# Optimization experiments

Hardware: AMD Instinct MI355X
Metric: run time of the kernel (lower is better)

The kernel has to match this reference:

```python
import jax, jax.numpy as jnp
import numpy as np

B, N, ND, ED = 4, 24, 13, 12          # batch, num_nodes, node feat dim, edge feat dim
H, NH, HD = 256, 8, 32                # hidden, heads, head dim (H == NH*HD)
L, T = 64, 1000                       # transformer layers, max_timestep
_SCALE = 1.0 / float(np.sqrt(H))      # torch divides by sqrt(node_dim)=sqrt(256)


def _ln(x, g, b):
    m = x.mean(-1, keepdims=True)
    v = ((x - m) ** 2).mean(-1, keepdims=True)
    return (x - m) / jnp.sqrt(v + 1e-5) * g + b


def setup_inputs() -> dict:
    key = jax.random.key(0)
    it = iter(jax.random.split(key, 40))
    def w(*s):
        return (jax.random.normal(next(it), s) * 0.02).astype(jnp.float32)
    z = lambda *s: jnp.zeros(s, jnp.float32)
    o = lambda *s: jnp.ones(s, jnp.float32)
    d = {}
    d['nodes'] = jax.random.normal(next(it), (B, N, ND), jnp.float32)
    d['edges'] = jax.random.normal(next(it), (B, N, N, ED), jnp.float32)
    d['conds'] = jax.random.randint(next(it), (B,), 0, T)
    # input MLPs
    d['inN_w1'] = w(ND, H); d['inN_b1'] = z(H); d['inN_w2'] = w(H, H); d['inN_b2'] = z(H)
    d['inE_w1'] = w(ED, H); d['inE_b1'] = z(H); d['inE_w2'] = w(H, H); d['inE_b2'] = z(H)
    d['inC_w1'] = w(T, H);  d['inC_b1'] = z(H); d['inC_w2'] = w(H, H); d['inC_b2'] = z(H)
    # stacked per-layer params (leading dim L, scanned)
    d['qkv_w'] = w(L, H, 3 * H); d['qkv_b'] = z(L, 3 * H)
    d['no_w'] = w(L, H, H); d['no_b'] = z(L, H)
    d['eo_w'] = w(L, H, H); d['eo_b'] = z(L, H)
    d['ln1n_g'] = o(L, H); d['ln1n_b'] = z(L, H)
    d['ln1e_g'] = o(L, H); d['ln1e_b'] = z(L, H)
    d['mn_w1'] = w(L, H, 4 * H); d['mn_b1'] = z(L, 4 * H)
    d['mn_w2'] = w(L, 4 * H, H); d['mn_b2'] = z(L, H)
    d['me_w1'] = w(L, H, 4 * H); d['me_b1'] = z(L, 4 * H)
    d['me_w2'] = w(L, 4 * H, H); d['me_b2'] = z(L, H)
    d['ln2n_g'] = o(L, H); d['ln2n_b'] = z(L, H)
    d['ln2e_g'] = o(L, H); d['ln2e_b'] = z(L, H)
    # output MLPs
    d['outN_w1'] = w(H, H); d['outN_b1'] = z(H); d['outN_w2'] = w(H, ND); d['outN_b2'] = z(ND)
    d['outE_w1'] = w(H, H); d['outE_b1'] = z(H); d['outE_w2'] = w(H, ED); d['outE_b2'] = z(ED)
    return d


def _forward(nodes, edges, conds,
             inN_w1, inN_b1, inN_w2, inN_b2, inE_w1, inE_b1, inE_w2, inE_b2,
             inC_w1, inC_b1, inC_w2, inC_b2,
             qkv_w, qkv_b, no_w, no_b, eo_w, eo_b,
             ln1n_g, ln1n_b, ln1e_g, ln1e_b,
             mn_w1, mn_b1, mn_w2, mn_b2, me_w1, me_b1, me_w2, me_b2,
             ln2n_g, ln2n_b, ln2e_g, ln2e_b,
             outN_w1, outN_b1, outN_w2, outN_b2, outE_w1, outE_b1, outE_w2, outE_b2):
    relu = jax.nn.relu
    c = jax.nn.one_hot(conds, T, dtype=nodes.dtype)
    c = relu(relu(c @ inC_w1 + inC_b1) @ inC_w2 + inC_b2)          # (B,H)
    n = relu(relu(nodes @ inN_w1 + inN_b1) @ inN_w2 + inN_b2)      # (B,N,H)
    e = relu(relu(edges @ inE_w1 + inE_b1) @ inE_w2 + inE_b2)      # (B,N,N,H)

    def layer(carry, p):
        n, e = carry
        (qw, qb, nw, nb, ew, eb, g1n, b1n, g1e, b1e,
         w1n, bb1n, w2n, bb2n, w1e, bb1e, w2e, bb2e, g2n, b2n, g2e, b2e) = p
        nc = n + c[:, None, :]
        q, k, v = jnp.split(nc @ qw + qb, 3, axis=-1)
        q = q.reshape(B, N, NH, HD); k = k.reshape(B, N, NH, HD); v = v.reshape(B, N, NH, HD)
        s5 = jnp.einsum('bihd,bjhd->bijhd', q, k) * _SCALE          # (B,N,N,NH,HD)
        ne5 = s5 + e.reshape(B, N, N, NH, HD)                       # edge-biased scores
        attn = jax.nn.softmax(ne5.sum(-1), axis=2)                  # (B,N,N,NH)
        wv = jnp.einsum('bijh,bjhd->bihd', attn, v).reshape(B, N, H)
        an = _ln(wv @ nw + nb + n, g1n, b1n)
        ae = _ln(relu(ne5.reshape(B, N, N, H) @ ew + eb) + e, g1e, b1e)
        n2 = _ln(relu(an @ w1n + bb1n) @ w2n + bb2n + an, g2n, b2n)
        e2 = _ln(relu(ae @ w1e + bb1e) @ w2e + bb2e + ae, g2e, b2e)
        return (n2, e2), None

    stacked = (qkv_w, qkv_b, no_w, no_b, eo_w, eo_b, ln1n_g, ln1n_b, ln1e_g, ln1e_b,
               mn_w1, mn_b1, mn_w2, mn_b2, me_w1, me_b1, me_w2, me_b2,
               ln2n_g, ln2n_b, ln2e_g, ln2e_b)
    (n, e), _ = jax.lax.scan(layer, (n, e), stacked)
    out_n = relu(n @ outN_w1 + outN_b1) @ outN_w2 + outN_b2
    out_e = relu(e @ outE_w1 + outE_b1) @ outE_w2 + outE_b2
    return out_n, out_e


def reference(nodes, edges, conds,
              inN_w1, inN_b1, inN_w2, inN_b2, inE_w1, inE_b1, inE_w2, inE_b2,
              inC_w1, inC_b1, inC_w2, inC_b2,
              qkv_w, qkv_b, no_w, no_b, eo_w, eo_b,
              ln1n_g, ln1n_b, ln1e_g, ln1e_b,
              mn_w1, mn_b1, mn_w2, mn_b2, me_w1, me_b1, me_w2, me_b2,
              ln2n_g, ln2n_b, ln2e_g, ln2e_b,
              outN_w1, outN_b1, outN_w2, outN_b2, outE_w1, outE_b1, outE_w2, outE_b2):
    return _forward(nodes, edges, conds,
                    inN_w1, inN_b1, inN_w2, inN_b2, inE_w1, inE_b1, inE_w2, inE_b2,
                    inC_w1, inC_b1, inC_w2, inC_b2,
                    qkv_w, qkv_b, no_w, no_b, eo_w, eo_b,
                    ln1n_g, ln1n_b, ln1e_g, ln1e_b,
                    mn_w1, mn_b1, mn_w2, mn_b2, me_w1, me_b1, me_w2, me_b2,
                    ln2n_g, ln2n_b, ln2e_g, ln2e_b,
                    outN_w1, outN_b1, outN_w2, outN_b2, outE_w1, outE_b1, outE_w2, outE_b2)
```

## Files before the change

### kernel.cpp

```cpp
#include <hip/hip_runtime.h>

typedef _Float16 half_t;
typedef _Float16 f16x8 __attribute__((ext_vector_type(8)));
typedef _Float16 f16x4 __attribute__((ext_vector_type(4)));
typedef float f32x4 __attribute__((ext_vector_type(4)));

#define BB 4
#define NNODE 24
#define NLAYER 64
#define SCALE_QK 0.0625f

#define WS_C     0
#define WS_N     1024
#define WS_NACC  25600
#define NACC_STRIDE 24576
#define WS_E     74752
#define WS_AE32  664576
#define WS_AE16  1254400
#define WS_AN16  1549312
#define WS_EPART 1561600
#define EPART_SLICE 589824
#define WS_WTF   3920896
#define SLOT_F16 1376256
#define OFF_QKVT 0
// ... 259 lines not shown
      int r = idx >> 8, col = idx & 255;
      float s = p.inN_b1[col];
      for (int kk = 0; kk < 13; ++kk) s += nd[r * 16 + kk] * p.inN_w1[kk * 256 + col];
      t1[r * 257 + col] = fmaxf(s, 0.f);
    }
    __syncthreads();
    {
      int col = tid & 255, rh = tid >> 8;
      float a6[6] = {0.f, 0.f, 0.f, 0.f, 0.f, 0.f};
      for (int k = 0; k < 256; ++k) {
        float w = p.inN_w2[(size_t)k * 256 + col];
#pragma unroll
        for (int r = 0; r < 6; ++r) a6[r] += t1[(rh * 6 + r) * 257 + k] * w;
      }
#pragma unroll
      for (int r = 0; r < 6; ++r) {
        int row = rh * 6 + r;
        n0[(size_t)(b * NNODE + i0 + row) * 256 + col] = fmaxf(a6[r] + p.inN_b2[col], 0.f);
      }
    }
  }
}

__global__ __launch_bounds__(512, 2) void k_attn(Params p, int lyr) {
  __shared__ __align__(16) char smem[90752];
  const int bid = blockIdx.x, tid = threadIdx.x;
  const int lane = tid & 63, wv = tid >> 6, l15 = lane & 15, kg = lane >> 4;
  float* ws = p.ws;
  half_t* wt = (half_t*)(ws + WS_WTF);
  const half_t* slot = wt + (size_t)(lyr % 3) * SLOT_F16;

  if (bid >= 96) {
    if (lyr + 2 < NLAYER) {
      half_t* dslot = wt + (size_t)((lyr + 2) % 3) * SLOT_F16;
      for (int tile = bid - 96; tile < 336; tile += 126)
        conv_layer_tile(p, dslot, lyr + 2, tile, smem);
    }
    return;
  }
  const int b = bid / NNODE, i = bid % NNODE;
  const size_t rowbase = (size_t)(b * NNODE + i) * NNODE;
  char* nc16 = smem;
  half_t* kv16 = (half_t*)(smem + 16384);
  half_t* qi16 = (half_t*)(smem + 40960);
  char* ne5 = smem + 41472;
  float* e32a = (float*)(smem + 57856);
  float* psum = (float*)(smem + 82816);
  float* sc = (float*)(smem + 85888);
  float* wvl = (float*)(smem + 86656);
  float* ni = (float*)(smem + 87680);
  float* anr = (float*)(smem + 88704);
  float* ae32 = ws + WS_AE32;
  half_t* ae16g = (half_t*)(ws + WS_AE16);
  const half_t* epart = (const half_t*)(ws + WS_EPART);
  const float* nacc_in = ws + WS_NACC + ((lyr + 1) & 1) * NACC_STRIDE;
  float* nacc_out = ws + WS_NACC + (lyr & 1) * NACC_STRIDE;
  const float* cb = ws + WS_C + b * 256;

  f16x8 pa0[8], pa1[8];
  f32x4 aa0[2], aa1[2];
  {
    const int r0_ = tid >> 5, k00 = (tid & 31) * 8;
    const size_t row0 = rowbase + r0_;
    if (lyr == 0) {
      aa0[0] = *(const f32x4*)(ws + WS_E + row0 * 256 + k00);
      aa0[1] = *(const f32x4*)(ws + WS_E + row0 * 256 + k00 + 4);
    } else {
      aa0[0] = *(const f32x4*)(ae32 + row0 * 256 + k00);
      aa0[1] = *(const f32x4*)(ae32 + row0 * 256 + k00 + 4);
#pragma unroll
      for (int hb = 0; hb < 8; ++hb)
        pa0[hb] = *(const f16x8*)(epart + (size_t)hb * EPART_SLICE + row0 * 256 + k00);
    }
    if (tid < 256) {
      const int r1_ = 16 + (tid >> 5);
      const size_t row1 = rowbase + r1_;
      if (lyr == 0) {
        aa1[0] = *(const f32x4*)(ws + WS_E + row1 * 256 + k00);
        aa1[1] = *(const f32x4*)(ws + WS_E + row1 * 256 + k00 + 4);
      } else {
        aa1[0] = *(const f32x4*)(ae32 + row1 * 256 + k00);
        aa1[1] = *(const f32x4*)(ae32 + row1 * 256 + k00 + 4);
#pragma unroll
        for (int hb = 0; hb < 8; ++hb)
          pa1[hb] = *(const f16x8*)(epart + (size_t)hb * EPART_SLICE + row1 * 256 + k00);
      }
    }
  }

  for (int r = wv; r < 32; r += 8) {
    const int c = lane * 4;
    f16x4 hv;
    if (r < NNODE) {
      f32x4 y;
      if (lyr == 0) {
        y = *(const f32x4*)(ws + WS_N + (size_t)(b * NNODE + r) * 256 + c);
      } else {
        f32x4 x = *(const f32x4*)(nacc_in + (size_t)(b * NNODE + r) * 256 + c);
        float s = x[0] + x[1] + x[2] + x[3];
        float s2 = x[0]*x[0] + x[1]*x[1] + x[2]*x[2] + x[3]*x[3];
#pragma unroll
        for (int off = 32; off; off >>= 1) { s += __shfl_xor(s, off); s2 += __shfl_xor(s2, off); }
        float mean = s * (1.f / 256.f);
        float rstd = rsqrtf(s2 * (1.f / 256.f) - mean * mean + 1e-5f);
        const float* g = p.ln2n_g + (size_t)(lyr - 1) * 256;
        const float* bv = p.ln2n_b + (size_t)(lyr - 1) * 256;
#pragma unroll
        for (int j = 0; j < 4; ++j) y[j] = (x[j] - mean) * rstd * g[c + j] + bv[c + j];
      }
      if (r == i) *(f32x4*)(ni + c) = y;
#pragma unroll
      for (int j = 0; j < 4; ++j) hv[j] = (half_t)(y[j] + cb[c + j]);
    } else {
#pragma unroll
      for (int j = 0; j < 4; ++j) hv[j] = (half_t)0.f;
    }
    *(f16x4*)(nc16 + r * 512 + ((lane * 8) ^ ((r & 7) << 4))) = hv;
  }
  __syncthreads();
  {
    const float* qb = p.qkv_b + (size_t)lyr * 768;
    gemm_rs<2, 8, 2, 256>(slot + OFF_QKVT, 256, nc16,
      [&](int nt, int m, f32x4 v) {
        const int col = (nt * 8 + wv) * 16 + l15;
        const float bc = qb[col];
#pragma unroll
        for (int r4 = 0; r4 < 4; ++r4) {
          const int row = m * 16 + kg * 4 + r4;
          if (row == i) qi16[col] = (half_t)(v[r4] + bc);
        }
      });
    gemm_rs<2, 8, 2, 256>(slot + OFF_QKVT + (size_t)256 * 256, 256, nc16,
      [&](int nt, int m, f32x4 v) {
        const int col = (nt * 8 + wv) * 16 + l15;
        const float bc = qb[256 + col];
#pragma unroll
        for (int r4 = 0; r4 < 4; ++r4) {
          const int row = m * 16 + kg * 4 + r4;
          if (row < NNODE) kv16[(size_t)row * 512 + col] = (half_t)(v[r4] + bc);
        }
      });
    gemm_rs<2, 8, 2, 256>(slot + OFF_QKVT + (size_t)512 * 256, 256, nc16,
      [&](int nt, int m, f32x4 v) {
        const int col = (nt * 8 + wv) * 16 + l15;
        const float bc = qb[512 + col];
#pragma unroll
        for (int r4 = 0; r4 < 4; ++r4) {
          const int row = m * 16 + kg * 4 + r4;
          if (row < NNODE) kv16[(size_t)row * 512 + 256 + col] = (half_t)(v[r4] + bc);
        }
      });
  }
  __syncthreads();
  {
    const float* gE = (lyr > 0) ? p.ln2e_g + (size_t)(lyr - 1) * 256 : nullptr;
    const float* bE = (lyr > 0) ? p.ln2e_b + (size_t)(lyr - 1) * 256 : nullptr;
    const float* mb2 = (lyr > 0) ? p.me_b2 + (size_t)(lyr - 1) * 256 : nullptr;
    {
      const int r = tid >> 5, k0 = (tid & 31) * 8;
      float x[8];
#pragma unroll
      for (int j = 0; j < 4; ++j) { x[j] = aa0[0][j]; x[4 + j] = aa0[1][j]; }
      if (lyr > 0) {
#pragma unroll
        for (int j = 0; j < 8; ++j) x[j] += mb2[k0 + j];
#pragma unroll
        for (int hb = 0; hb < 8; ++hb)
#pragma unroll
          for (int j = 0; j < 8; ++j) x[j] += (float)pa0[hb][j];
        float s = 0.f, s2 = 0.f;
#pragma unroll
        for (int j = 0; j < 8; ++j) { s += x[j]; s2 += x[j] * x[j]; }
#pragma unroll
        for (int off = 16; off; off >>= 1) { s += __shfl_xor(s, off); s2 += __shfl_xor(s2, off); }
        float mean = s * (1.f / 256.f);
        float rstd = rsqrtf(s2 * (1.f / 256.f) - mean * mean + 1e-5f);
#pragma unroll
        for (int j = 0; j < 8; ++j) x[j] = (x[j] - mean) * rstd * gE[k0 + j] + bE[k0 + j];
      }
      f16x8 q8 = *(const f16x8*)(qi16 + k0);
      f16x8 k8 = *(const f16x8*)(kv16 + (size_t)r * 512 + k0);
      f16x8 v;
      float ps = 0.f;
#pragma unroll
      for (int j = 0; j < 8; ++j) {
        float f = SCALE_QK * (float)q8[j] * (float)k8[j] + x[j];
        v[j] = (half_t)f;
        ps += f;
        e32a[r * 260 + k0 + j] = x[j];
      }
      psum[r * 32 + (tid & 31)] = ps;
      *(f16x8*)(ne5 + r * 512 + ((k0 * 2) ^ ((r & 7) << 4))) = v;
    }
    {
      const int idx = 512 + tid;
      const int r = idx >> 5, k0 = (idx & 31) * 8;
      if (r < NNODE) {
        float x[8];
#pragma unroll
        for (int j = 0; j < 4; ++j) { x[j] = aa1[0][j]; x[4 + j] = aa1[1][j]; }
        if (lyr > 0) {
#pragma unroll
          for (int j = 0; j < 8; ++j) x[j] += mb2[k0 + j];
#pragma unroll
          for (int hb = 0; hb < 8; ++hb)
#pragma unroll
            for (int j = 0; j < 8; ++j) x[j] += (float)pa1[hb][j];
          float s = 0.f, s2 = 0.f;
#pragma unroll
          for (int j = 0; j < 8; ++j) { s += x[j]; s2 += x[j] * x[j]; }
#pragma unroll
          for (int off = 16; off; off >>= 1) { s += __shfl_xor(s, off); s2 += __shfl_xor(s2, off); }
          float mean = s * (1.f / 256.f);
          float rstd = rsqrtf(s2 * (1.f / 256.f) - mean * mean + 1e-5f);
#pragma unroll
          for (int j = 0; j < 8; ++j) x[j] = (x[j] - mean) * rstd * gE[k0 + j] + bE[k0 + j];
        }
        f16x8 q8 = *(const f16x8*)(qi16 + k0);
        f16x8 k8 = *(const f16x8*)(kv16 + (size_t)r * 512 + k0);
        f16x8 v;
        float ps = 0.f;
#pragma unroll
        for (int j = 0; j < 8; ++j) {
          float f = SCALE_QK * (float)q8[j] * (float)k8[j] + x[j];
          v[j] = (half_t)f;
          ps += f;
          e32a[r * 260 + k0 + j] = x[j];
        }
        psum[r * 32 + (idx & 31)] = ps;
        *(f16x8*)(ne5 + r * 512 + ((k0 * 2) ^ ((r & 7) << 4))) = v;
      } else {
        f16x8 z;
#pragma unroll
        for (int j = 0; j < 8; ++j) z[j] = (half_t)0.f;
        *(f16x8*)(ne5 + r * 512 + ((k0 * 2) ^ ((r & 7) << 4))) = z;
      }
    }
  }
  __syncthreads();
  if (tid < 192) {
    int hq = tid & 7;
    sc[tid] = psum[(tid >> 3) * 32 + hq * 4] + psum[(tid >> 3) * 32 + hq * 4 + 1] +
              psum[(tid >> 3) * 32 + hq * 4 + 2] + psum[(tid >> 3) * 32 + hq * 4 + 3];
  }
  __syncthreads();
  if (tid < 8) {
    const int h = tid;
    float mx = -1e30f;
#pragma unroll
    for (int j = 0; j < 24; ++j) mx = fmaxf(mx, sc[j * 8 + h]);
    float ex[24]; float ssum = 0.f;
#pragma unroll
    for (int j = 0; j < 24; ++j) { ex[j] = __expf(sc[j * 8 + h] - mx); ssum += ex[j]; }
    float inv = 1.f / ssum;
#pragma unroll
    for (int j = 0; j < 24; ++j) sc[j * 8 + h] = ex[j] * inv;
  }
  __syncthreads();
  if (tid < 256) {
    const int d = tid, h = d >> 5;
    float a = 0.f;
#pragma unroll
    for (int j = 0; j < 24; ++j) a += sc[j * 8 + h] * (float)kv16[(size_t)j * 512 + 256 + d];
    wvl[d] = a;
  }
  {
    const float* eob = p.eo_b + (size_t)lyr * 256;
    gemm_rs<2, 8, 2, 256>(slot + OFF_EOT, 256, ne5,
      [&](int nt, int m, f32x4 v) {
        const int col = (nt * 8 + wv) * 16 + l15;
#pragma unroll
        for (int r4 = 0; r4 < 4; ++r4) {
          const int row = m * 16 + kg * 4 + r4;
          if (row < NNODE)
            e32a[row * 260 + col] = fmaxf(v[r4] + eob[col], 0.f) + e32a[row * 260 + col];
        }
      });
  }
  __syncthreads();
  {
    const float* g = p.ln1e_g + (size_t)lyr * 256;
    const float* bv = p.ln1e_b + (size_t)lyr * 256;
    for (int r = wv; r < NNODE; r += 8) {
      float x[4];
#pragma unroll
      for (int j = 0; j < 4; ++j) x[j] = e32a[r * 260 + lane * 4 + j];
      float s = x[0] + x[1] + x[2] + x[3];
      float s2 = x[0]*x[0] + x[1]*x[1] + x[2]*x[2] + x[3]*x[3];
#pragma unroll
      for (int off = 32; off; off >>= 1) { s += __shfl_xor(s, off); s2 += __shfl_xor(s2, off); }
      float mean = s * (1.f / 256.f);
      float rstd = rsqrtf(s2 * (1.f / 256.f) - mean * mean + 1e-5f);
      f16x4 hv; f32x4 yv;
#pragma unroll
      for (int j = 0; j < 4; ++j) {
        int c = lane * 4 + j;
        float y = (x[j] - mean) * rstd * g[c] + bv[c];
        yv[j] = y; hv[j] = (half_t)y;
      }
      *(f32x4*)(ae32 + (rowbase + r) * 256 + lane * 4) = yv;
      *(f16x4*)(ae16g + (rowbase + r) * 256 + lane * 4) = hv;
    }
  }
  {
    const half_t* NOT_ = slot + OFF_NOT;
    int c = tid & 255, hf = tid >> 8;
    float s = 0.f;
    const half_t* wp = NOT_ + (size_t)c * 256 + hf * 128;
#pragma unroll
    for (int k8 = 0; k8 < 16; ++k8) {
      f16x8 w8 = *(const f16x8*)(wp + k8 * 8);
#pragma unroll
      for (int j = 0; j < 8; ++j) s += wvl[hf * 128 + k8 * 8 + j] * (float)w8[j];
    }
    anr[hf * 256 + c] = s;
  }
  __syncthreads();
  if (wv == 0) {
    const float* nob = p.no_b + (size_t)lyr * 256;
    const float* g = p.ln1n_g + (size_t)lyr * 256;
    const float* bv = p.ln1n_b + (size_t)lyr * 256;
    const float* mb2 = p.mn_b2 + (size_t)lyr * 256;
    float x[4];
#pragma unroll
    for (int j = 0; j < 4; ++j) {
      int c = lane * 4 + j;
      x[j] = anr[c] + anr[256 + c] + nob[c] + ni[c];
    }
    float s = x[0] + x[1] + x[2] + x[3];
    float s2 = x[0]*x[0] + x[1]*x[1] + x[2]*x[2] + x[3]*x[3];
#pragma unroll
    for (int off = 32; off; off >>= 1) { s += __shfl_xor(s, off); s2 += __shfl_xor(s2, off); }
    float mean = s * (1.f / 256.f);
    float rstd = rsqrtf(s2 * (1.f / 256.f) - mean * mean + 1e-5f);
    f16x4 hv; f32x4 av;
#pragma unroll
    for (int j = 0; j < 4; ++j) {
      int c = lane * 4 + j;
      float y = (x[j] - mean) * rstd * g[c] + bv[c];
      hv[j] = (half_t)y;
      av[j] = y + mb2[c];
    }
    *(f16x4*)((half_t*)(ws + WS_AN16) + (size_t)(b * NNODE + i) * 256 + lane * 4) = hv;
    *(f32x4*)(nacc_out + (size_t)(b * NNODE + i) * 256 + lane * 4) = av;
  }
}

__global__ __launch_bounds__(512, 2) void k_mlp(Params p, int lyr) {
  __shared__ __align__(16) char smem[73728];
  const int bid = blockIdx.x, tid = threadIdx.x;
  const int lane = tid & 63, wv = tid >> 6, l15 = lane & 15, kg = lane >> 4;
  float* ws = p.ws;
  half_t* wt = (half_t*)(ws + WS_WTF);
  const half_t* slot = wt + (size_t)(lyr % 3) * SLOT_F16;

  if (bid < 192) {
    const int rb = bid >> 3, hb = bid & 7;
    const int row0 = rb * 96;
    char* A16 = smem;
    char* hl = smem + 49152;
    f16x8 b1[8];
    load_b1<8>(slot + OFF_ME1T + (size_t)(hb * 128) * 256, 256, b1);
    const half_t* aeg = (const half_t*)(ws + WS_AE16) + (size_t)row0 * 256;
    for (int idx = tid; idx < 96 * 32; idx += 512) {
      int r = idx >> 5, c8 = idx & 31;
      f16x8 v = *(const f16x8*)(aeg + r * 256 + c8 * 8);
      *(f16x8*)(A16 + r * 512 + ((c8 * 16) ^ ((r & 7) << 4))) = v;
    }
    __syncthreads();
    const float* mb1 = p.me_b1 + (size_t)lyr * 1024 + hb * 128;
    gemm_rs_preb<8, 6, 256>(b1, A16,
      [&](int m, f32x4 v) {
        const int colb = wv * 16 + l15;
        const float bc = mb1[colb];
#pragma unroll
        for (int r4 = 0; r4 < 4; ++r4) {
          const int row = m * 16 + kg * 4 + r4;
          *(half_t*)(hl + row * 256 + ((colb * 2) ^ ((row & 7) << 4))) = (half_t)fmaxf(v[r4] + bc, 0.f);
        }
      });
    __syncthreads();
    half_t* ep = (half_t*)(ws + WS_EPART) + (size_t)hb * EPART_SLICE + (size_t)row0 * 256;
    gemm_rs<2, 4, 6, 128>(slot + OFF_ME2T + hb * 128, 1024, hl,
      [&](int nt, int m, f32x4 v) {
        const int col = (nt * 8 + wv) * 16 + l15;
#pragma unroll
        for (int r4 = 0; r4 < 4; ++r4)
          ep[(size_t)(m * 16 + kg * 4 + r4) * 256 + col] = (half_t)v[r4];
      });
  } else {
    const int hb = bid - 192;
    char* A16 = smem;
    char* hl = smem + 49152;
    f16x8 b1[8];
    load_b1<8>(slot + OFF_MN1T + (size_t)(hb * 128) * 256, 256, b1);
    const half_t* ang = (const half_t*)(ws + WS_AN16);
    for (int idx = tid; idx < 96 * 32; idx += 512) {
      int r = idx >> 5, c8 = idx & 31;
      f16x8 v = *(const f16x8*)(ang + (size_t)r * 256 + c8 * 8);
      *(f16x8*)(A16 + r * 512 + ((c8 * 16) ^ ((r & 7) << 4))) = v;
    }
    __syncthreads();
    const float* mb1 = p.mn_b1 + (size_t)lyr * 1024 + hb * 128;
    gemm_rs_preb<8, 6, 256>(b1, A16,
      [&](int m, f32x4 v) {
        const int colb = wv * 16 + l15;
        const float bc = mb1[colb];
#pragma unroll
        for (int r4 = 0; r4 < 4; ++r4) {
          const int row = m * 16 + kg * 4 + r4;
          *(half_t*)(hl + row * 256 + ((colb * 2) ^ ((row & 7) << 4))) = (half_t)fmaxf(v[r4] + bc, 0.f);
        }
      });
    __syncthreads();
    float* nacc_out = ws + WS_NACC + (lyr & 1) * NACC_STRIDE;
    gemm_rs<2, 4, 6, 128>(slot + OFF_MN2T + hb * 128, 1024, hl,
      [&](int nt, int m, f32x4 v) {
        const int col = (nt * 8 + wv) * 16 + l15;
#pragma unroll
        for (int r4 = 0; r4 < 4; ++r4)
          atomicAdd(&nacc_out[(size_t)(m * 16 + kg * 4 + r4) * 256 + col], v[r4]);
      });
  }
}

__global__ __launch_bounds__(512, 2) void k_out(Params p) {
  __shared__ __align__(16) char smem[49472];
  const int bid = blockIdx.x, tid = threadIdx.x;
  const int lane = tid & 63, wv = tid >> 6, l15 = lane & 15, kg = lane >> 4;
  float* ws = p.ws;
  half_t* wt = (half_t*)(ws + WS_WTF);
  const float* ae32 = ws + WS_AE32;
  const half_t* epart = (const half_t*)(ws + WS_EPART);
  if (bid < 96) {
    const int b = bid / NNODE, i = bid % NNODE;
    const size_t rowbase = (size_t)(b * NNODE + i) * NNODE;
    char* A16 = smem;
    float* h2f = (float*)(smem + 16384);
    const float* mb2 = p.me_b2 + (size_t)63 * 256;
    const float* g = p.ln2e_g + (size_t)63 * 256;
    const float* bvv = p.ln2e_b + (size_t)63 * 256;
    for (int idx = tid; idx < 32 * 32; idx += 512) {
      int r = idx >> 5, kb = idx & 31, k0 = kb * 8;
      f16x8 v;
#pragma unroll
// ... 90 lines not shown

extern "C" void kernel_launch(void* const* d_in, const int* in_sizes, int n_in,
                              void* d_out, int out_size, void* d_ws, size_t ws_size,
                              hipStream_t stream) {
  (void)in_sizes; (void)n_in; (void)out_size; (void)ws_size;
  Params p;
  const float* const* fi = (const float* const*)d_in;
  p.nodes = fi[0]; p.edges = fi[1]; p.conds = (const int*)d_in[2];
  p.inN_w1 = fi[3]; p.inN_b1 = fi[4]; p.inN_w2 = fi[5]; p.inN_b2 = fi[6];
  p.inE_w1 = fi[7]; p.inE_b1 = fi[8]; p.inE_w2 = fi[9]; p.inE_b2 = fi[10];
  p.inC_w1 = fi[11]; p.inC_b1 = fi[12]; p.inC_w2 = fi[13]; p.inC_b2 = fi[14];
  p.qkv_w = fi[15]; p.qkv_b = fi[16]; p.no_w = fi[17]; p.no_b = fi[18];
  p.eo_w = fi[19]; p.eo_b = fi[20];
  p.ln1n_g = fi[21]; p.ln1n_b = fi[22]; p.ln1e_g = fi[23]; p.ln1e_b = fi[24];
  p.mn_w1 = fi[25]; p.mn_b1 = fi[26]; p.mn_w2 = fi[27]; p.mn_b2 = fi[28];
  p.me_w1 = fi[29]; p.me_b1 = fi[30]; p.me_w2 = fi[31]; p.me_b2 = fi[32];
  p.ln2n_g = fi[33]; p.ln2n_b = fi[34]; p.ln2e_g = fi[35]; p.ln2e_b = fi[36];
  p.outN_w1 = fi[37]; p.outN_b1 = fi[38]; p.outN_w2 = fi[39]; p.outN_b2 = fi[40];
  p.outE_w1 = fi[41]; p.outE_b1 = fi[42]; p.outE_w2 = fi[43]; p.outE_b2 = fi[44];
  p.ws = (float*)d_ws; p.out = (float*)d_out;

  k_embedA<<<dim3(132), dim3(512), 0, stream>>>(p);
  k_embedB<<<dim3(104), dim3(512), 0, stream>>>(p);
  for (int l = 0; l < NLAYER; ++l) {
    k_attn<<<dim3(222), dim3(512), 0, stream>>>(p, l);
    k_mlp<<<dim3(200), dim3(512), 0, stream>>>(p, l);
  }
  k_out<<<dim3(104), dim3(512), 0, stream>>>(p);
}
```

Baseline: 3.060 ms.

## Fuse per-layer attention and MLP kernels into one persistent cooperative kernel

Replaces the 128 per-layer kernel launches (attention and MLP for each of 64 layers) with a single cooperative kernel of 256 blocks. It loops over layers and uses grid-wide syncs between the attention and MLP phases. The edge-row prefetch loads move after the QKV GEMM, which cuts shared memory and register pressure, and the weight-conversion work spreads over 160 blocks. This removes launch and kernel-boundary overhead at the cost of grid.sync latency, and it needs all 256 blocks to be co-resident.

```diff
diff --git a/kernel.cpp b/kernel.cpp
--- a/kernel.cpp
+++ b/kernel.cpp
@@ -1,4 +1,7 @@
 #include <hip/hip_runtime.h>
+#include <hip/hip_cooperative_groups.h>
+
+namespace cg = cooperative_groups;
 
 typedef _Float16 half_t;
 typedef _Float16 f16x8 __attribute__((ext_vector_type(8)));
@@ -305,405 +308,390 @@
   }
 }
 
-__global__ __launch_bounds__(512, 2) void k_attn(Params p, int lyr) {
-  __shared__ __align__(16) char smem[90752];
+__global__ __launch_bounds__(512, 2) void k_layers(Params p) {
+  __shared__ __align__(16) char smem[87680];
+  cg::grid_group grid = cg::this_grid();
   const int bid = blockIdx.x, tid = threadIdx.x;
   const int lane = tid & 63, wv = tid >> 6, l15 = lane & 15, kg = lane >> 4;
   float* ws = p.ws;
   half_t* wt = (half_t*)(ws + WS_WTF);
-  const half_t* slot = wt + (size_t)(lyr % 3) * SLOT_F16;
-
-  if (bid >= 96) {
-    if (lyr + 2 < NLAYER) {
-      half_t* dslot = wt + (size_t)((lyr + 2) % 3) * SLOT_F16;
-      for (int tile = bid - 96; tile < 336; tile += 126)
-        conv_layer_tile(p, dslot, lyr + 2, tile, smem);
-    }
-    return;
-  }
-  const int b = bid / NNODE, i = bid % NNODE;
-  const size_t rowbase = (size_t)(b * NNODE + i) * NNODE;
-  char* nc16 = smem;
-  half_t* kv16 = (half_t*)(smem + 16384);
-  half_t* qi16 = (half_t*)(smem + 40960);
-  char* ne5 = smem + 41472;
-  float* e32a = (float*)(smem + 57856);
-  float* psum = (float*)(smem + 82816);
-  float* sc = (float*)(smem + 85888);
-  float* wvl = (float*)(smem + 86656);
-  float* ni = (float*)(smem + 87680);
-  float* anr = (float*)(smem + 88704);
   float* ae32 = ws + WS_AE32;
   half_t* ae16g = (half_t*)(ws + WS_AE16);
-  const half_t* epart = (const half_t*)(ws + WS_EPART);
-  const float* nacc_in = ws + WS_NACC + ((lyr + 1) & 1) * NACC_STRIDE;
-  float* nacc_out = ws + WS_NACC + (lyr & 1) * NACC_STRIDE;
-  const float* cb = ws + WS_C + b * 256;
-
-  f16x8 pa0[8], pa1[8];
-  f32x4 aa0[2], aa1[2];
-  {
-    const int r0_ = tid >> 5, k00 = (tid & 31) * 8;
-    const size_t row0 = rowbase + r0_;
-    if (lyr == 0) {
-      aa0[0] = *(const f32x4*)(ws + WS_E + row0 * 256 + k00);
-      aa0[1] = *(const f32x4*)(ws + WS_E + row0 * 256 + k00 + 4);
-    } else {
-      aa0[0] = *(const f32x4*)(ae32 + row0 * 256 + k00);
-      aa0[1] = *(const f32x4*)(ae32 + row0 * 256 + k00 + 4);
-#pragma unroll
-      for (int hb = 0; hb < 8; ++hb)
-        pa0[hb] = *(const f16x8*)(epart + (size_t)hb * EPART_SLICE + row0 * 256 + k00);
-    }
-    if (tid < 256) {
-      const int r1_ = 16 + (tid >> 5);
-      const size_t row1 = rowbase + r1_;
-      if (lyr == 0) {
-        aa1[0] = *(const f32x4*)(ws + WS_E + row1 * 256 + k00);
-        aa1[1] = *(const f32x4*)(ws + WS_E + row1 * 256 + k00 + 4);
-      } else {
-        aa1[0] = *(const f32x4*)(ae32 + row1 * 256 + k00);
-        aa1[1] = *(const f32x4*)(ae32 + row1 * 256 + k00 + 4);
-#pragma unroll
-        for (int hb = 0; hb < 8; ++hb)
-          pa1[hb] = *(const f16x8*)(epart + (size_t)hb * EPART_SLICE + row1 * 256 + k00);
-      }
-    }
-  }
-
-  for (int r = wv; r < 32; r += 8) {
-    const int c = lane * 4;
-    f16x4 hv;
-    if (r < NNODE) {
-      f32x4 y;
-      if (lyr == 0) {
-        y = *(const f32x4*)(ws + WS_N + (size_t)(b * NNODE + r) * 256 + c);
-      } else {
-        f32x4 x = *(const f32x4*)(nacc_in + (size_t)(b * NNODE + r) * 256 + c);
+  const half_t* epart_c = (const half_t*)(ws + WS_EPART);
+
+  for (int lyr = 0; lyr < NLAYER; ++lyr) {
+    const half_t* slot = wt + (size_t)(lyr % 3) * SLOT_F16;
+    const float* nacc_in = ws + WS_NACC + ((lyr + 1) & 1) * NACC_STRIDE;
+    float* nacc_out = ws + WS_NACC + (lyr & 1) * NACC_STRIDE;
+
+    if (bid < 96) {
+      const int b = bid / NNODE, i = bid % NNODE;
+      const size_t rowbase = (size_t)(b * NNODE + i) * NNODE;
+      char* nc16 = smem;
+      half_t* kv16 = (half_t*)(smem + 16384);
+      half_t* qi16 = (half_t*)(smem + 40960);
+      char* ne5 = smem + 41472;
+      float* e32a = (float*)(smem + 57856);
+      float* sc = (float*)(smem + 82816);
+      float* wvl = (float*)(smem + 83584);
+      float* ni = (float*)(smem + 84608);
+      float* anr = (float*)(smem + 85632);
+      const float* cb = ws + WS_C + b * 256;
+
+      for (int r = wv; r < 32; r += 8) {
+        const int c = lane * 4;
+        f16x4 hv;
+        if (r < NNODE) {
+          f32x4 y;
+          if (lyr == 0) {
+            y = *(const f32x4*)(ws + WS_N + (size_t)(b * NNODE + r) * 256 + c);
+          } else {
+            f32x4 x = *(const f32x4*)(nacc_in + (size_t)(b * NNODE + r) * 256 + c);
+            float s = x[0] + x[1] + x[2] + x[3];
+            float s2 = x[0]*x[0] + x[1]*x[1] + x[2]*x[2] + x[3]*x[3];
+#pragma unroll
+            for (int off = 32; off; off >>= 1) { s += __shfl_xor(s, off); s2 += __shfl_xor(s2, off); }
+            float mean = s * (1.f / 256.f);
+            float rstd = rsqrtf(s2 * (1.f / 256.f) - mean * mean + 1e-5f);
+            const float* g = p.ln2n_g + (size_t)(lyr - 1) * 256;
+            const float* bv = p.ln2n_b + (size_t)(lyr - 1) * 256;
+#pragma unroll
+            for (int j = 0; j < 4; ++j) y[j] = (x[j] - mean) * rstd * g[c + j] + bv[c + j];
+          }
+          if (r == i) *(f32x4*)(ni + c) = y;
+#pragma unroll
+          for (int j = 0; j < 4; ++j) hv[j] = (half_t)(y[j] + cb[c + j]);
+        } else {
+#pragma unroll
+          for (int j = 0; j < 4; ++j) hv[j] = (half_t)0.f;
+        }
+        *(f16x4*)(nc16 + r * 512 + ((lane * 8) ^ ((r & 7) << 4))) = hv;
+      }
+      __syncthreads();
+      {
+        const float* qb = p.qkv_b + (size_t)lyr * 768;
+        gemm_rs<2, 8, 2, 256>(slot + OFF_QKVT, 256, nc16,
+          [&](int nt, int m, f32x4 v) {
+            const int col = (nt * 8 + wv) * 16 + l15;
+            const float bc = qb[col];
+#pragma unroll
+            for (int r4 = 0; r4 < 4; ++r4) {
+              const int row = m * 16 + kg * 4 + r4;
+              if (row == i) qi16[col] = (half_t)(v[r4] + bc);
+            }
+          });
+        gemm_rs<2, 8, 2, 256>(slot + OFF_QKVT + (size_t)256 * 256, 256, nc16,
+          [&](int nt, int m, f32x4 v) {
+            const int col = (nt * 8 + wv) * 16 + l15;
+            const float bc = qb[256 + col];
+#pragma unroll
+            for (int r4 = 0; r4 < 4; ++r4) {
+              const int row = m * 16 + kg * 4 + r4;
+              if (row < NNODE) kv16[(size_t)row * 512 + col] = (half_t)(v[r4] + bc);
+            }
+          });
+        gemm_rs<2, 8, 2, 256>(slot + OFF_QKVT + (size_t)512 * 256, 256, nc16,
+          [&](int nt, int m, f32x4 v) {
+            const int col = (nt * 8 + wv) * 16 + l15;
+            const float bc = qb[512 + col];
+#pragma unroll
+            for (int r4 = 0; r4 < 4; ++r4) {
+              const int row = m * 16 + kg * 4 + r4;
+              if (row < NNODE) kv16[(size_t)row * 512 + 256 + col] = (half_t)(v[r4] + bc);
+            }
+          });
+      }
+      __syncthreads();
+      {
+        const float* gE = (lyr > 0) ? p.ln2e_g + (size_t)(lyr - 1) * 256 : nullptr;
+        const float* bE = (lyr > 0) ? p.ln2e_b + (size_t)(lyr - 1) * 256 : nullptr;
+        const float* mb2 = (lyr > 0) ? p.me_b2 + (size_t)(lyr - 1) * 256 : nullptr;
+        const int r0_ = tid >> 5, kb = tid & 31, k00 = kb * 8;
+        const int r1_ = 16 + r0_;
+        const size_t row0 = rowbase + r0_;
+        const size_t row1 = rowbase + r1_;
+        const bool has1 = (r1_ < NNODE);
+        f32x4 aa0[2], aa1[2]; f16x8 pa0[8], pa1[8];
+        if (lyr == 0) {
+          aa0[0] = *(const f32x4*)(ws + WS_E + row0 * 256 + k00);
+          aa0[1] = *(const f32x4*)(ws + WS_E + row0 * 256 + k00 + 4);
+          if (has1) {
+            aa1[0] = *(const f32x4*)(ws + WS_E + row1 * 256 + k00);
+            aa1[1] = *(const f32x4*)(ws + WS_E + row1 * 256 + k00 + 4);
+          }
+        } else {
+          aa0[0] = *(const f32x4*)(ae32 + row0 * 256 + k00);
+          aa0[1] = *(const f32x4*)(ae32 + row0 * 256 + k00 + 4);
+#pragma unroll
+          for (int hb = 0; hb < 8; ++hb)
+            pa0[hb] = *(const f16x8*)(epart_c + (size_t)hb * EPART_SLICE + row0 * 256 + k00);
+          if (has1) {
+            aa1[0] = *(const f32x4*)(ae32 + row1 * 256 + k00);
+            aa1[1] = *(const f32x4*)(ae32 + row1 * 256 + k00 + 4);
+#pragma unroll
+            for (int hb = 0; hb < 8; ++hb)
+              pa1[hb] = *(const f16x8*)(epart_c + (size_t)hb * EPART_SLICE + row1 * 256 + k00);
+          }
+        }
+        f16x8 q8 = *(const f16x8*)(qi16 + k00);
+        {
+          float x[8];
+#pragma unroll
+          for (int j = 0; j < 4; ++j) { x[j] = aa0[0][j]; x[4 + j] = aa0[1][j]; }
+          if (lyr > 0) {
+#pragma unroll
+            for (int j = 0; j < 8; ++j) x[j] += mb2[k00 + j];
+#pragma unroll
+            for (int hb = 0; hb < 8; ++hb)
+#pragma unroll
+              for (int j = 0; j < 8; ++j) x[j] += (float)pa0[hb][j];
+            float s = 0.f, s2 = 0.f;
+#pragma unroll
+            for (int j = 0; j < 8; ++j) { s += x[j]; s2 += x[j] * x[j]; }
+#pragma unroll
+            for (int off = 16; off; off >>= 1) { s += __shfl_xor(s, off); s2 += __shfl_xor(s2, off); }
+            float mean = s * (1.f / 256.f);
+            float rstd = rsqrtf(s2 * (1.f / 256.f) - mean * mean + 1e-5f);
+#pragma unroll
+            for (int j = 0; j < 8; ++j) x[j] = (x[j] - mean) * rstd * gE[k00 + j] + bE[k00 + j];
+          }
+          f16x8 k8 = *(const f16x8*)(kv16 + (size_t)r0_ * 512 + k00);
+          f16x8 v;
+          float ps = 0.f;
+#pragma unroll
+          for (int j = 0; j < 8; ++j) {
+            float f = SCALE_QK * (float)q8[j] * (float)k8[j] + x[j];
+            v[j] = (half_t)f;
+            ps += f;
+            e32a[r0_ * 260 + k00 + j] = x[j];
+          }
+          float hs = ps + __shfl_xor(ps, 1);
+          hs += __shfl_xor(hs, 2);
+          if ((kb & 3) == 0) sc[r0_ * 8 + (kb >> 2)] = hs;
+          *(f16x8*)(ne5 + r0_ * 512 + ((k00 * 2) ^ ((r0_ & 7) << 4))) = v;
+        }
+        if (has1) {
+          float x[8];
+#pragma unroll
+          for (int j = 0; j < 4; ++j) { x[j] = aa1[0][j]; x[4 + j] = aa1[1][j]; }
+          if (lyr > 0) {
+#pragma unroll
+            for (int j = 0; j < 8; ++j) x[j] += mb2[k00 + j];
+#pragma unroll
+            for (int hb = 0; hb < 8; ++hb)
+#pragma unroll
+              for (int j = 0; j < 8; ++j) x[j] += (float)pa1[hb][j];
+            float s = 0.f, s2 = 0.f;
+#pragma unroll
+            for (int j = 0; j < 8; ++j) { s += x[j]; s2 += x[j] * x[j]; }
+#pragma unroll
+            for (int off = 16; off; off >>= 1) { s += __shfl_xor(s, off); s2 += __shfl_xor(s2, off); }
+            float mean = s * (1.f / 256.f);
+            float rstd = rsqrtf(s2 * (1.f / 256.f) - mean * mean + 1e-5f);
+#pragma unroll
+            for (int j = 0; j < 8; ++j) x[j] = (x[j] - mean) * rstd * gE[k00 + j] + bE[k00 + j];
+          }
+          f16x8 k8 = *(const f16x8*)(kv16 + (size_t)r1_ * 512 + k00);
+          f16x8 v;
+          float ps = 0.f;
+#pragma unroll
+          for (int j = 0; j < 8; ++j) {
+            float f = SCALE_QK * (float)q8[j] * (float)k8[j] + x[j];
+            v[j] = (half_t)f;
+            ps += f;
+            e32a[r1_ * 260 + k00 + j] = x[j];
+          }
+          float hs = ps + __shfl_xor(ps, 1);
+          hs += __shfl_xor(hs, 2);
+          if ((kb & 3) == 0) sc[r1_ * 8 + (kb >> 2)] = hs;
+          *(f16x8*)(ne5 + r1_ * 512 + ((k00 * 2) ^ ((r1_ & 7) << 4))) = v;
+        } else {
+          f16x8 z;
+#pragma unroll
+          for (int j = 0; j < 8; ++j) z[j] = (half_t)0.f;
+          *(f16x8*)(ne5 + r1_ * 512 + ((k00 * 2) ^ ((r1_ & 7) << 4))) = z;
+        }
+      }
+      __syncthreads();
+      if (tid < 256) {
+        const int h = tid >> 5, j = tid & 31;
+        float v = (j < 24) ? sc[j * 8 + h] : -1e30f;
+        float mx = v;
+#pragma unroll
+        for (int off = 16; off; off >>= 1) mx = fmaxf(mx, __shfl_xor(mx, off));
+        float ex = (j < 24) ? __expf(v - mx) : 0.f;
+        float sum = ex;
+#pragma unroll
+        for (int off = 16; off; off >>= 1) sum += __shfl_xor(sum, off);
+        if (j < 24) sc[j * 8 + h] = ex / sum;
+      }
+      __syncthreads();
+      if (tid < 256) {
+        const int d = tid, h = d >> 5;
+        float a = 0.f;
+#pragma unroll
+        for (int j = 0; j < 24; ++j) a += sc[j * 8 + h] * (float)kv16[(size_t)j * 512 + 256 + d];
+        wvl[d] = a;
+      }
+      {
+        const float* eob = p.eo_b + (size_t)lyr * 256;
+        gemm_rs<2, 8, 2, 256>(slot + OFF_EOT, 256, ne5,
+          [&](int nt, int m, f32x4 v) {
+            const int col = (nt * 8 + wv) * 16 + l15;
+#pragma unroll
+            for (int r4 = 0; r4 < 4; ++r4) {
+              const int row = m * 16 + kg * 4 + r4;
+              if (row < NNODE)
+                e32a[row * 260 + col] = fmaxf(v[r4] + eob[col], 0.f) + e32a[row * 260 + col];
+            }
+          });
+      }
+      __syncthreads();
+      {
+        const float* g = p.ln1e_g + (size_t)lyr * 256;
+        const float* bv = p.ln1e_b + (size_t)lyr * 256;
+        for (int r = wv; r < NNODE; r += 8) {
+          float x[4];
+#pragma unroll
+          for (int j = 0; j < 4; ++j) x[j] = e32a[r * 260 + lane * 4 + j];
+          float s = x[0] + x[1] + x[2] + x[3];
+          float s2 = x[0]*x[0] + x[1]*x[1] + x[2]*x[2] + x[3]*x[3];
+#pragma unroll
+          for (int off = 32; off; off >>= 1) { s += __shfl_xor(s, off); s2 += __shfl_xor(s2, off); }
+          float mean = s * (1.f / 256.f);
+          float rstd = rsqrtf(s2 * (1.f / 256.f) - mean * mean + 1e-5f);
+          f16x4 hv; f32x4 yv;
+#pragma unroll
+          for (int j = 0; j < 4; ++j) {
+            int c = lane * 4 + j;
+            float y = (x[j] - mean) * rstd * g[c] + bv[c];
+            yv[j] = y; hv[j] = (half_t)y;
+          }
+          *(f32x4*)(ae32 + (rowbase + r) * 256 + lane * 4) = yv;
+          *(f16x4*)(ae16g + (rowbase + r) * 256 + lane * 4) = hv;
+        }
+      }
+      {
+        const half_t* NOT_ = slot + OFF_NOT;
+        int c = tid & 255, hf = tid >> 8;
+        float s = 0.f;
+        const half_t* wp = NOT_ + (size_t)c * 256 + hf * 128;
+#pragma unroll
+        for (int k8 = 0; k8 < 16; ++k8) {
+          f16x8 w8 = *(const f16x8*)(wp + k8 * 8);
+#pragma unroll
+          for (int j = 0; j < 8; ++j) s += wvl[hf * 128 + k8 * 8 + j] * (float)w8[j];
+        }
+        anr[hf * 256 + c] = s;
+      }
+      __syncthreads();
+      if (wv == 0) {
+        const float* nob = p.no_b + (size_t)lyr * 256;
+        const float* g = p.ln1n_g + (size_t)lyr * 256;
+        const float* bv = p.ln1n_b + (size_t)lyr * 256;
+        const float* mb2n = p.mn_b2 + (size_t)lyr * 256;
+        float x[4];
+#pragma unroll
+        for (int j = 0; j < 4; ++j) {
+          int c = lane * 4 + j;
+          x[j] = anr[c] + anr[256 + c] + nob[c] + ni[c];
+        }
         float s = x[0] + x[1] + x[2] + x[3];
         float s2 = x[0]*x[0] + x[1]*x[1] + x[2]*x[2] + x[3]*x[3];
 #pragma unroll
         for (int off = 32; off; off >>= 1) { s += __shfl_xor(s, off); s2 += __shfl_xor(s2, off); }
         float mean = s * (1.f / 256.f);
         float rstd = rsqrtf(s2 * (1.f / 256.f) - mean * mean + 1e-5f);
-        const float* g = p.ln2n_g + (size_t)(lyr - 1) * 256;
-        const float* bv = p.ln2n_b + (size_t)(lyr - 1) * 256;
-#pragma unroll
-        for (int j = 0; j < 4; ++j) y[j] = (x[j] - mean) * rstd * g[c + j] + bv[c + j];
-      }
-      if (r == i) *(f32x4*)(ni + c) = y;
-#pragma unroll
-      for (int j = 0; j < 4; ++j) hv[j] = (half_t)(y[j] + cb[c + j]);
+        f16x4 hv; f32x4 av;
+#pragma unroll
+        for (int j = 0; j < 4; ++j) {
+          int c = lane * 4 + j;
+          float y = (x[j] - mean) * rstd * g[c] + bv[c];
+          hv[j] = (half_t)y;
+          av[j] = y + mb2n[c];
+        }
+        *(f16x4*)((half_t*)(ws + WS_AN16) + (size_t)(b * NNODE + i) * 256 + lane * 4) = hv;
+        *(f32x4*)(nacc_out + (size_t)(b * NNODE + i) * 256 + lane * 4) = av;
+      }
     } else {
-#pragma unroll
-      for (int j = 0; j < 4; ++j) hv[j] = (half_t)0.f;
-    }
-    *(f16x4*)(nc16 + r * 512 + ((lane * 8) ^ ((r & 7) << 4))) = hv;
-  }
-  __syncthreads();
-  {
-    const float* qb = p.qkv_b + (size_t)lyr * 768;
-    gemm_rs<2, 8, 2, 256>(slot + OFF_QKVT, 256, nc16,
-      [&](int nt, int m, f32x4 v) {
-        const int col = (nt * 8 + wv) * 16 + l15;
-        const float bc = qb[col];
-#pragma unroll
-        for (int r4 = 0; r4 < 4; ++r4) {
-          const int row = m * 16 + kg * 4 + r4;
-          if (row == i) qi16[col] = (half_t)(v[r4] + bc);
-        }
-      });
-    gemm_rs<2, 8, 2, 256>(slot + OFF_QKVT + (size_t)256 * 256, 256, nc16,
-      [&](int nt, int m, f32x4 v) {
-        const int col = (nt * 8 + wv) * 16 + l15;
-        const float bc = qb[256 + col];
-#pragma unroll
-        for (int r4 = 0; r4 < 4; ++r4) {
-          const int row = m * 16 + kg * 4 + r4;
-          if (row < NNODE) kv16[(size_t)row * 512 + col] = (half_t)(v[r4] + bc);
-        }
-      });
-    gemm_rs<2, 8, 2, 256>(slot + OFF_QKVT + (size_t)512 * 256, 256, nc16,
-      [&](int nt, int m, f32x4 v) {
-        const int col = (nt * 8 + wv) * 16 + l15;
-        const float bc = qb[512 + col];
-#pragma unroll
-        for (int r4 = 0; r4 < 4; ++r4) {
-          const int row = m * 16 + kg * 4 + r4;
-          if (row < NNODE) kv16[(size_t)row * 512 + 256 + col] = (half_t)(v[r4] + bc);
-        }
-      });
-  }
-  __syncthreads();
-  {
-    const float* gE = (lyr > 0) ? p.ln2e_g + (size_t)(lyr - 1) * 256 : nullptr;
-    const float* bE = (lyr > 0) ? p.ln2e_b + (size_t)(lyr - 1) * 256 : nullptr;
-    const float* mb2 = (lyr > 0) ? p.me_b2 + (size_t)(lyr - 1) * 256 : nullptr;
-    {
-      const int r = tid >> 5, k0 = (tid & 31) * 8;
-      float x[8];
-#pragma unroll
-      for (int j = 0; j < 4; ++j) { x[j] = aa0[0][j]; x[4 + j] = aa0[1][j]; }
-      if (lyr > 0) {
-#pragma unroll
-        for (int j = 0; j < 8; ++j) x[j] += mb2[k0 + j];
-#pragma unroll
-        for (int hb = 0; hb < 8; ++hb)
-#pragma unroll
-          for (int j = 0; j < 8; ++j) x[j] += (float)pa0[hb][j];
-        float s = 0.f, s2 = 0.f;
-#pragma unroll
-        for (int j = 0; j < 8; ++j) { s += x[j]; s2 += x[j] * x[j]; }
-#pragma unroll
-        for (int off = 16; off; off >>= 1) { s += __shfl_xor(s, off); s2 += __shfl_xor(s2, off); }
-        float mean = s * (1.f / 256.f);
-        float rstd = rsqrtf(s2 * (1.f / 256.f) - mean * mean + 1e-5f);
-#pragma unroll
-        for (int j = 0; j < 8; ++j) x[j] = (x[j] - mean) * rstd * gE[k0 + j] + bE[k0 + j];
-      }
-      f16x8 q8 = *(const f16x8*)(qi16 + k0);
-      f16x8 k8 = *(const f16x8*)(kv16 + (size_t)r * 512 + k0);
-      f16x8 v;
-      float ps = 0.f;
-#pragma unroll
-      for (int j = 0; j < 8; ++j) {
-        float f = SCALE_QK * (float)q8[j] * (float)k8[j] + x[j];
-        v[j] = (half_t)f;
-        ps += f;
-        e32a[r * 260 + k0 + j] = x[j];
-      }
-      psum[r * 32 + (tid & 31)] = ps;
-      *(f16x8*)(ne5 + r * 512 + ((k0 * 2) ^ ((r & 7) << 4))) = v;
-    }
-    {
-      const int idx = 512 + tid;
-      const int r = idx >> 5, k0 = (idx & 31) * 8;
-      if (r < NNODE) {
-        float x[8];
-#pragma unroll
-        for (int j = 0; j < 4; ++j) { x[j] = aa1[0][j]; x[4 + j] = aa1[1][j]; }
-        if (lyr > 0) {
-#pragma unroll
-          for (int j = 0; j < 8; ++j) x[j] += mb2[k0 + j];
-#pragma unroll
-          for (int hb = 0; hb < 8; ++hb)
-#pragma unroll
-            for (int j = 0; j < 8; ++j) x[j] += (float)pa1[hb][j];
-          float s = 0.f, s2 = 0.f;
-#pragma unroll
-          for (int j = 0; j < 8; ++j) { s += x[j]; s2 += x[j] * x[j]; }
-#pragma unroll
-          for (int off = 16; off; off >>= 1) { s += __shfl_xor(s, off); s2 += __shfl_xor(s2, off); }
-          float mean = s * (1.f / 256.f);
-          float rstd = rsqrtf(s2 * (1.f / 256.f) - mean * mean + 1e-5f);
-#pragma unroll
-          for (int j = 0; j < 8; ++j) x[j] = (x[j] - mean) * rstd * gE[k0 + j] + bE[k0 + j];
-        }
-        f16x8 q8 = *(const f16x8*)(qi16 + k0);
-        f16x8 k8 = *(const f16x8*)(kv16 + (size_t)r * 512 + k0);
-        f16x8 v;
-        float ps = 0.f;
-#pragma unroll
-        for (int j = 0; j < 8; ++j) {
-          float f = SCALE_QK * (float)q8[j] * (float)k8[j] + x[j];
-          v[j] = (half_t)f;
-          ps += f;
-          e32a[r * 260 + k0 + j] = x[j];
-        }
-        psum[r * 32 + (idx & 31)] = ps;
-        *(f16x8*)(ne5 + r * 512 + ((k0 * 2) ^ ((r & 7) << 4))) = v;
-      } else {
-        f16x8 z;
-#pragma unroll
-        for (int j = 0; j < 8; ++j) z[j] = (half_t)0.f;
-        *(f16x8*)(ne5 + r * 512 + ((k0 * 2) ^ ((r & 7) << 4))) = z;
-      }
-    }
-  }
-  __syncthreads();
-  if (tid < 192) {
-    int hq = tid & 7;
-    sc[tid] = psum[(tid >> 3) * 32 + hq * 4] + psum[(tid >> 3) * 32 + hq * 4 + 1] +
-              psum[(tid >> 3) * 32 + hq * 4 + 2] + psum[(tid >> 3) * 32 + hq * 4 + 3];
-  }
-  __syncthreads();
-  if (tid < 8) {
-    const int h = tid;
-    float mx = -1e30f;
-#pragma unroll
-    for (int j = 0; j < 24; ++j) mx = fmaxf(mx, sc[j * 8 + h]);
-    float ex[24]; float ssum = 0.f;
-#pragma unroll
-    for (int j = 0; j < 24; ++j) { ex[j] = __expf(sc[j * 8 + h] - mx); ssum += ex[j]; }
-    float inv = 1.f / ssum;
-#pragma unroll
-    for (int j = 0; j < 24; ++j) sc[j * 8 + h] = ex[j] * inv;
-  }
-  __syncthreads();
-  if (tid < 256) {
-    const int d = tid, h = d >> 5;
-    float a = 0.f;
-#pragma unroll
-    for (int j = 0; j < 24; ++j) a += sc[j * 8 + h] * (float)kv16[(size_t)j * 512 + 256 + d];
-    wvl[d] = a;
-  }
-  {
-    const float* eob = p.eo_b + (size_t)lyr * 256;
-    gemm_rs<2, 8, 2, 256>(slot + OFF_EOT, 256, ne5,
-      [&](int nt, int m, f32x4 v) {
-        const int col = (nt * 8 + wv) * 16 + l15;
-#pragma unroll
-        for (int r4 = 0; r4 < 4; ++r4) {
-          const int row = m * 16 + kg * 4 + r4;
-          if (row < NNODE)
-            e32a[row * 260 + col] = fmaxf(v[r4] + eob[col], 0.f) + e32a[row * 260 + col];
-        }
-      });
-  }
-  __syncthreads();
-  {
-    const float* g = p.ln1e_g + (size_t)lyr * 256;
-    const float* bv = p.ln1e_b + (size_t)lyr * 256;
-    for (int r = wv; r < NNODE; r += 8) {
-      float x[4];
-#pragma unroll
-      for (int j = 0; j < 4; ++j) x[j] = e32a[r * 260 + lane * 4 + j];
-      float s = x[0] + x[1] + x[2] + x[3];
-      float s2 = x[0]*x[0] + x[1]*x[1] + x[2]*x[2] + x[3]*x[3];
-#pragma unroll
-      for (int off = 32; off; off >>= 1) { s += __shfl_xor(s, off); s2 += __shfl_xor(s2, off); }
-      float mean = s * (1.f / 256.f);
-      float rstd = rsqrtf(s2 * (1.f / 256.f) - mean * mean + 1e-5f);
-      f16x4 hv; f32x4 yv;
-#pragma unroll
-      for (int j = 0; j < 4; ++j) {
-        int c = lane * 4 + j;
-        float y = (x[j] - mean) * rstd * g[c] + bv[c];
-        yv[j] = y; hv[j] = (half_t)y;
-      }
-      *(f32x4*)(ae32 + (rowbase + r) * 256 + lane * 4) = yv;
-      *(f16x4*)(ae16g + (rowbase + r) * 256 + lane * 4) = hv;
-    }
-  }
-  {
-    const half_t* NOT_ = slot + OFF_NOT;
-    int c = tid & 255, hf = tid >> 8;
-    float s = 0.f;
-    const half_t* wp = NOT_ + (size_t)c * 256 + hf * 128;
-#pragma unroll
-    for (int k8 = 0; k8 < 16; ++k8) {
-      f16x8 w8 = *(const f16x8*)(wp + k8 * 8);
-#pragma unroll
-      for (int j = 0; j < 8; ++j) s += wvl[hf * 128 + k8 * 8 + j] * (float)w8[j];
-    }
-    anr[hf * 256 + c] = s;
-  }
-  __syncthreads();
-  if (wv == 0) {
-    const float* nob = p.no_b + (size_t)lyr * 256;
-    const float* g = p.ln1n_g + (size_t)lyr * 256;
-    const float* bv = p.ln1n_b + (size_t)lyr * 256;
-    const float* mb2 = p.mn_b2 + (size_t)lyr * 256;
-    float x[4];
-#pragma unroll
-    for (int j = 0; j < 4; ++j) {
-      int c = lane * 4 + j;
-      x[j] = anr[c] + anr[256 + c] + nob[c] + ni[c];
-    }
-    float s = x[0] + x[1] + x[2] + x[3];
-    float s2 = x[0]*x[0] + x[1]*x[1] + x[2]*x[2] + x[3]*x[3];
-#pragma unroll
-    for (int off = 32; off; off >>= 1) { s += __shfl_xor(s, off); s2 += __shfl_xor(s2, off); }
-    float mean = s * (1.f / 256.f);
-    float rstd = rsqrtf(s2 * (1.f / 256.f) - mean * mean + 1e-5f);
-    f16x4 hv; f32x4 av;
-#pragma unroll
-    for (int j = 0; j < 4; ++j) {
-      int c = lane * 4 + j;
-      float y = (x[j] - mean) * rstd * g[c] + bv[c];
-      hv[j] = (half_t)y;
-      av[j] = y + mb2[c];
-    }
-    *(f16x4*)((half_t*)(ws + WS_AN16) + (size_t)(b * NNODE + i) * 256 + lane * 4) = hv;
-    *(f32x4*)(nacc_out + (size_t)(b * NNODE + i) * 256 + lane * 4) = av;
-  }
-}
-
-__global__ __launch_bounds__(512, 2) void k_mlp(Params p, int lyr) {
-  __shared__ __align__(16) char smem[73728];
-  const int bid = blockIdx.x, tid = threadIdx.x;
-  const int lane = tid & 63, wv = tid >> 6, l15 = lane & 15, kg = lane >> 4;
-  float* ws = p.ws;
-  half_t* wt = (half_t*)(ws + WS_WTF);
-  const half_t* slot = wt + (size_t)(lyr % 3) * SLOT_F16;
-
-  if (bid < 192) {
-    const int rb = bid >> 3, hb = bid & 7;
-    const int row0 = rb * 96;
-    char* A16 = smem;
-    char* hl = smem + 49152;
-    f16x8 b1[8];
-    load_b1<8>(slot + OFF_ME1T + (size_t)(hb * 128) * 256, 256, b1);
-    const half_t* aeg = (const half_t*)(ws + WS_AE16) + (size_t)row0 * 256;
-    for (int idx = tid; idx < 96 * 32; idx += 512) {
-      int r = idx >> 5, c8 = idx & 31;
-      f16x8 v = *(const f16x8*)(aeg + r * 256 + c8 * 8);
-      *(f16x8*)(A16 + r * 512 + ((c8 * 16) ^ ((r & 7) << 4))) = v;
-    }
-    __syncthreads();
-    const float* mb1 = p.me_b1 + (size_t)lyr * 1024 + hb * 128;
-    gemm_rs_preb<8, 6, 256>(b1, A16,
-      [&](int m, f32x4 v) {
-        const int colb = wv * 16 + l15;
-        const float bc = mb1[colb];
-#pragma unroll
-        for (int r4 = 0; r4 < 4; ++r4) {
-          const int row = m * 16 + kg * 4 + r4;
-          *(half_t*)(hl + row * 256 + ((colb * 2) ^ ((row & 7) << 4))) = (half_t)fmaxf(v[r4] + bc, 0.f);
-        }
-      });
-    __syncthreads();
-    half_t* ep = (half_t*)(ws + WS_EPART) + (size_t)hb * EPART_SLICE + (size_t)row0 * 256;
-    gemm_rs<2, 4, 6, 128>(slot + OFF_ME2T + hb * 128, 1024, hl,
-      [&](int nt, int m, f32x4 v) {
-        const int col = (nt * 8 + wv) * 16 + l15;
-#pragma unroll
-        for (int r4 = 0; r4 < 4; ++r4)
-          ep[(size_t)(m * 16 + kg * 4 + r4) * 256 + col] = (half_t)v[r4];
-      });
-  } else {
-    const int hb = bid - 192;
-    char* A16 = smem;
-    char* hl = smem + 49152;
-    f16x8 b1[8];
-    load_b1<8>(slot + OFF_MN1T + (size_t)(hb * 128) * 256, 256, b1);
-    const half_t* ang = (const half_t*)(ws + WS_AN16);
-    for (int idx = tid; idx < 96 * 32; idx += 512) {
-      int r = idx >> 5, c8 = idx & 31;
-      f16x8 v = *(const f16x8*)(ang + (size_t)r * 256 + c8 * 8);
-      *(f16x8*)(A16 + r * 512 + ((c8 * 16) ^ ((r & 7) << 4))) = v;
-    }
-    __syncthreads();
-    const float* mb1 = p.mn_b1 + (size_t)lyr * 1024 + hb * 128;
-    gemm_rs_preb<8, 6, 256>(b1, A16,
-      [&](int m, f32x4 v) {
-        const int colb = wv * 16 + l15;
-        const float bc = mb1[colb];
-#pragma unroll
-        for (int r4 = 0; r4 < 4; ++r4) {
-          const int row = m * 16 + kg * 4 + r4;
-          *(half_t*)(hl + row * 256 + ((colb * 2) ^ ((row & 7) << 4))) = (half_t)fmaxf(v[r4] + bc, 0.f);
-        }
-      });
-    __syncthreads();
-    float* nacc_out = ws + WS_NACC + (lyr & 1) * NACC_STRIDE;
-    gemm_rs<2, 4, 6, 128>(slot + OFF_MN2T + hb * 128, 1024, hl,
-      [&](int nt, int m, f32x4 v) {
-        const int col = (nt * 8 + wv) * 16 + l15;
-#pragma unroll
-        for (int r4 = 0; r4 < 4; ++r4)
-          atomicAdd(&nacc_out[(size_t)(m * 16 + kg * 4 + r4) * 256 + col], v[r4]);
-      });
+      if (lyr + 2 < NLAYER) {
+        half_t* dslot = wt + (size_t)((lyr + 2) % 3) * SLOT_F16;
+        for (int tile = bid - 96; tile < 336; tile += 160)
+          conv_layer_tile(p, dslot, lyr + 2, tile, smem);
+      }
+    }
+    grid.sync();
+
+    if (bid < 192) {
+      const int rb = bid >> 3, hb = bid & 7;
+      const int row0 = rb * 96;
+      char* A16 = smem;
+      char* hl = smem + 49152;
+      f16x8 b1[8];
+      load_b1<8>(slot + OFF_ME1T + (size_t)(hb * 128) * 256, 256, b1);
+      const half_t* aeg = ae16g + (size_t)row0 * 256;
+      for (int idx = tid; idx < 96 * 32; idx += 512) {
+        int r = idx >> 5, c8 = idx & 31;
+        f16x8 v = *(const f16x8*)(aeg + r * 256 + c8 * 8);
+        *(f16x8*)(A16 + r * 512 + ((c8 * 16) ^ ((r & 7) << 4))) = v;
+      }
+      __syncthreads();
+      const float* mb1 = p.me_b1 + (size_t)lyr * 1024 + hb * 128;
+      gemm_rs_preb<8, 6, 256>(b1, A16,
+        [&](int m, f32x4 v) {
+          const int colb = wv * 16 + l15;
+          const float bc = mb1[colb];
+#pragma unroll
+          for (int r4 = 0; r4 < 4; ++r4) {
+            const int row = m * 16 + kg * 4 + r4;
+            *(half_t*)(hl + row * 256 + ((colb * 2) ^ ((row & 7) << 4))) = (half_t)fmaxf(v[r4] + bc, 0.f);
+          }
+        });
+      __syncthreads();
+      half_t* ep = (half_t*)(ws + WS_EPART) + (size_t)hb * EPART_SLICE + (size_t)row0 * 256;
+      gemm_rs<2, 4, 6, 128>(slot + OFF_ME2T + hb * 128, 1024, hl,
+        [&](int nt, int m, f32x4 v) {
+          const int col = (nt * 8 + wv) * 16 + l15;
+#pragma unroll
+          for (int r4 = 0; r4 < 4; ++r4)
+            ep[(size_t)(m * 16 + kg * 4 + r4) * 256 + col] = (half_t)v[r4];
+        });
+      __syncthreads();
+    } else if (bid < 200) {
+      const int hb = bid - 192;
+      char* A16 = smem;
+      char* hl = smem + 49152;
+      f16x8 b1[8];
+      load_b1<8>(slot + OFF_MN1T + (size_t)(hb * 128) * 256, 256, b1);
+      const half_t* ang = (const half_t*)(ws + WS_AN16);
+      for (int idx = tid; idx < 96 * 32; idx += 512) {
+        int r = idx >> 5, c8 = idx & 31;
+        f16x8 v = *(const f16x8*)(ang + (size_t)r * 256 + c8 * 8);
+        *(f16x8*)(A16 + r * 512 + ((c8 * 16) ^ ((r & 7) << 4))) = v;
+      }
+      __syncthreads();
+      const float* mb1 = p.mn_b1 + (size_t)lyr * 1024 + hb * 128;
+      gemm_rs_preb<8, 6, 256>(b1, A16,
+        [&](int m, f32x4 v) {
+          const int colb = wv * 16 + l15;
+          const float bc = mb1[colb];
+#pragma unroll
+          for (int r4 = 0; r4 < 4; ++r4) {
+            const int row = m * 16 + kg * 4 + r4;
+            *(half_t*)(hl + row * 256 + ((colb * 2) ^ ((row & 7) << 4))) = (half_t)fmaxf(v[r4] + bc, 0.f);
+          }
+        });
+      __syncthreads();
+      gemm_rs<2, 4, 6, 128>(slot + OFF_MN2T + hb * 128, 1024, hl,
+        [&](int nt, int m, f32x4 v) {
+          const int col = (nt * 8 + wv) * 16 + l15;
+#pragma unroll
+          for (int r4 = 0; r4 < 4; ++r4)
+            atomicAdd(&nacc_out[(size_t)(m * 16 + kg * 4 + r4) * 256 + col], v[r4]);
+        });
+      __syncthreads();
+    }
+    grid.sync();
   }
 }
 
@@ -840,9 +828,7 @@
 
   k_embedA<<<dim3(132), dim3(512), 0, stream>>>(p);
   k_embedB<<<dim3(104), dim3(512), 0, stream>>>(p);
-  for (int l = 0; l < NLAYER; ++l) {
-    k_attn<<<dim3(222), dim3(512), 0, stream>>>(p, l);
-    k_mlp<<<dim3(200), dim3(512), 0, stream>>>(p, l);
-  }
+  void* args[] = {(void*)&p};
+  hipLaunchCooperativeKernel((void*)k_layers, dim3(256), dim3(512), args, 0, stream);
   k_out<<<dim3(104), dim3(512), 0, stream>>>(p);
 }
```

New measurement: 8.047 ms. 2.63x slower.
